# Optimization experiments

Measured on AMD Instinct MI355X. Metric: run time of the kernel, lower is better.

Reference implementation:

```python
import jax, jax.numpy as jnp
import numpy as np

H = 16  # num_heads
EPS = 1e-5


def _ln(x, g, b):
    m = x.mean(-1, keepdims=True)
    v = x.var(-1, keepdims=True)
    return (x - m) / jnp.sqrt(v + EPS) * g + b


def _heads(x):
    b, s, d = x.shape
    return x.reshape(b, s, H, d // H).transpose(0, 2, 1, 3)  # [B,H,S,dh]


def _merge_buggy(z):
    # replicate torch view([B,H,S,dh] -> [B,S,H*dh]) WITHOUT head transpose
    b, h, s, dh = z.shape
    return z.reshape(b, s, h * dh)


def _attn(q_in, kv_in, resid, wq, bq, wk, bk, wv, bv, g, be, scale_by_seq, apply_triu):
    q = _heads(q_in @ wq + bq)
    k = _heads(kv_in @ wk + bk)
    v = _heads(kv_in @ wv + bv)
    qk = jnp.einsum('bhqd,bhkd->bhqk', q, k)
    qk = jnp.where(jnp.isnan(qk), -jnp.inf, qk)
    if scale_by_seq:
        qk = qk / jnp.sqrt(jnp.asarray(qk.shape[-1], qk.dtype))  # sqrt(seq_len), as in source
    a = jax.nn.softmax(qk, axis=-1)
    a = jnp.where(jnp.isnan(a), 0.0, a)
    v = jnp.where(jnp.isnan(v), 0.0, v)
    if apply_triu:
        s = a.shape[-1]
        a = a * jnp.triu(jnp.ones((s, s), a.dtype))  # post-softmax multiplicative mask
    z = jnp.einsum('bhqk,bhkd->bhqd', a, v)
    z = _merge_buggy(z)
    return _ln(resid + z, g, be)


def setup_inputs() -> dict:
    key = jax.random.key(0)
    ks = jax.random.split(key, 20)
    B, S, D, F = 2, 2048, 1024, 1024
    p = lambda k, sh: (jax.random.normal(k, sh, jnp.float32) * 0.02)
    inp = {
        'encoded': jax.random.normal(ks[0], (B, S, D), jnp.float32),
        'decoded': jax.random.normal(ks[1], (B, S, D), jnp.float32),
        'sa_wq': p(ks[2], (D, D)), 'sa_bq': jnp.zeros((D,), jnp.float32),
        'sa_wk': p(ks[3], (D, D)), 'sa_bk': jnp.zeros((D,), jnp.float32),
        'sa_wv': p(ks[4], (D, D)), 'sa_bv': jnp.zeros((D,), jnp.float32),
        'sa_g': jnp.ones((D,), jnp.float32), 'sa_b': jnp.zeros((D,), jnp.float32),
        'ca_wq': p(ks[5], (D, D)), 'ca_bq': jnp.zeros((D,), jnp.float32),
        'ca_wk': p(ks[6], (D, D)), 'ca_bk': jnp.zeros((D,), jnp.float32),
        'ca_wv': p(ks[7], (D, D)), 'ca_bv': jnp.zeros((D,), jnp.float32),
        'ca_g': jnp.ones((D,), jnp.float32), 'ca_b': jnp.zeros((D,), jnp.float32),
        'ffn_w1': p(ks[8], (D, F)), 'ffn_b1': jnp.zeros((F,), jnp.float32),
        'ffn_w2': p(ks[9], (F, D)), 'ffn_b2': jnp.zeros((D,), jnp.float32),
        'ffn_g': jnp.ones((D,), jnp.float32), 'ffn_b': jnp.zeros((D,), jnp.float32),
    }
    return inp


def reference(encoded, decoded,
              sa_wq, sa_bq, sa_wk, sa_bk, sa_wv, sa_bv, sa_g, sa_b,
              ca_wq, ca_bq, ca_wk, ca_bk, ca_wv, ca_bv, ca_g, ca_b,
              ffn_w1, ffn_b1, ffn_w2, ffn_b2, ffn_g, ffn_b):
    # masked self-attention (quirky: scale by sqrt(S), post-softmax triu mask)
    x = _attn(decoded, decoded, decoded, sa_wq, sa_bq, sa_wk, sa_bk, sa_wv, sa_bv,
              sa_g, sa_b, scale_by_seq=True, apply_triu=True)
    # cross-attention (no scale, no mask)
    x = _attn(x, encoded, x, ca_wq, ca_bq, ca_wk, ca_bk, ca_wv, ca_bv,
              ca_g, ca_b, scale_by_seq=False, apply_triu=False)
    # FFN with residual + LayerNorm (dropout = identity in eval)
    y = jax.nn.relu(x @ ffn_w1 + ffn_b1) @ ffn_w2 + ffn_b2
    return _ln(y + x, ffn_g, ffn_b)
```

## Files before the change

### kernel.cpp

```cpp
#include <hip/hip_runtime.h>
#include <hip/hip_bf16.h>
#include <cstdint>


typedef __attribute__((ext_vector_type(8))) short bf16x8;
typedef __attribute__((ext_vector_type(4))) float f32x4;
typedef unsigned short u16;

#define MFMA16(a, b, c) __builtin_amdgcn_mfma_f32_16x16x32_bf16((a), (b), (c), 0, 0, 0)

__device__ __forceinline__ u16 f2b(float f) {
    __hip_bfloat16 h = __float2bfloat16(f);
    return __builtin_bit_cast(u16, h);
}
__device__ __forceinline__ float b2f(u16 u) {
    return __builtin_bit_cast(float, (uint32_t)u << 16);
}
__device__ __forceinline__ void g2lds16(const u16* g, u16* l) {
    __builtin_amdgcn_global_load_lds((const __attribute__((address_space(1))) void*)g,
                                     (__attribute__((address_space(3))) void*)l, 16, 0, 0);
}

__global__ __launch_bounds__(256) void cast_bf16_kernel(const float* __restrict__ x,
                                                        u16* __restrict__ y, int n4) {
    int i = blockIdx.x * 256 + threadIdx.x;
    if (i >= n4) return;
    float4 v = reinterpret_cast<const float4*>(x)[i];
    ushort4 o;
    o.x = f2b(v.x); o.y = f2b(v.y); o.z = f2b(v.z); o.w = f2b(v.w);
    reinterpret_cast<ushort4*>(y)[i] = o;
}

__global__ __launch_bounds__(256) void wcast_all_kernel(
    const float* __restrict__ w0, const float* __restrict__ w1,
    const float* __restrict__ w2, const float* __restrict__ w3,
    const float* __restrict__ w4, const float* __restrict__ w5,
    const float* __restrict__ w6, const float* __restrict__ w7,
    u16* __restrict__ wt) {
    __shared__ float t[32][33];
    const float* W;
    switch (blockIdx.z) {
        case 0: W = w0; break; case 1: W = w1; break;
        case 2: W = w2; break; case 3: W = w3; break;
        case 4: W = w4; break; case 5: W = w5; break;
        case 6: W = w6; break; default: W = w7; break;
    }
    u16* Wt = wt + (size_t)blockIdx.z * 1048576;
    int tx = threadIdx.x & 31, ty = threadIdx.x >> 5;
    int bx = blockIdx.x * 32, by = blockIdx.y * 32;
#pragma unroll
    for (int j = 0; j < 4; ++j)
        t[ty + j * 8][tx] = W[(size_t)(by + ty + j * 8) * 1024 + bx + tx];
    __syncthreads();
#pragma unroll
    for (int j = 0; j < 4; ++j)
        Wt[(size_t)(bx + ty + j * 8) * 1024 + by + tx] = f2b(t[tx][ty + j * 8]);
}

__global__ __launch_bounds__(256) void vtrans_kernel(const u16* __restrict__ V,
                                                     u16* __restrict__ Vt) {
    __shared__ u16 t[32][34];
    const int tx = threadIdx.x & 31, ty = threadIdx.x >> 5;
    const int s0 = blockIdx.x * 32, d0 = blockIdx.y * 32, b = blockIdx.z;
    const u16* src = V + (size_t)b * 2048 * 1024;
    u16* dst = Vt + (size_t)b * 1024 * 2048;
#pragma unroll
    for (int j = 0; j < 4; ++j)
        t[ty + j * 8][tx] = src[(size_t)(s0 + ty + j * 8) * 1024 + d0 + tx];
    __syncthreads();
#pragma unroll
    for (int j = 0; j < 4; ++j)
        dst[(size_t)(d0 + ty + j * 8) * 2048 + s0 + tx] = t[tx][ty + j * 8];
}

__global__ __launch_bounds__(256) void gemm_kernel(
    const u16* __restrict__ A, const u16* __restrict__ Bt,
    const float* __restrict__ bias0, const float* __restrict__ bias1,
    const float* __restrict__ bias2,
    u16* __restrict__ o0, u16* __restrict__ o1, u16* __restrict__ o2,
    int K, int relu, float oscale0) {
    __shared__ __align__(16) u16 As[2][128][32];
    __shared__ __align__(16) u16 Bs[2][128][32];
    const int tid = threadIdx.x, lane = tid & 63, w = tid >> 6;
    const int wm = w >> 1, wn = w & 1, l15 = lane & 15, l4 = lane >> 4;
    const int bm = blockIdx.y * 128, bn = blockIdx.x * 128;
    const int srow = lane >> 2, sc = lane & 3;
    const int scs = (sc ^ (srow & 3)) * 8;
    const u16* aW = A + (size_t)(bm + w * 16 + srow) * K + scs;
    const u16* bW = Bt + (size_t)(bn + w * 16 + srow) * K + scs;
    f32x4 acc[4][4] = {};

#define GSTAGE(bf, kt)                                                  \
    do {                                                                \
        g2lds16(aW + (kt), &As[bf][w * 16][0]);                         \
        g2lds16(aW + (size_t)64 * K + (kt), &As[bf][64 + w * 16][0]);   \
        g2lds16(bW + (kt), &Bs[bf][w * 16][0]);                         \
        g2lds16(bW + (size_t)64 * K + (kt), &Bs[bf][64 + w * 16][0]);   \
    } while (0)

    const int nt = K / 32;
    GSTAGE(0, 0);
    for (int t = 0; t < nt; ++t) {
        __syncthreads();
        if (t + 1 < nt) GSTAGE((t + 1) & 1, (t + 1) * 32);
        const int bf = t & 1;
        bf16x8 af[4], bfr[4];
#pragma unroll
        for (int m = 0; m < 4; ++m) {
            int row = wm * 64 + m * 16 + l15;
            af[m] = *reinterpret_cast<const bf16x8*>(&As[bf][row][(l4 ^ (l15 & 3)) * 8]);
        }
#pragma unroll
        for (int n = 0; n < 4; ++n) {
            int row = wn * 64 + n * 16 + l15;
            bfr[n] = *reinterpret_cast<const bf16x8*>(&Bs[bf][row][(l4 ^ (l15 & 3)) * 8]);
        }
        __builtin_amdgcn_s_setprio(1);
#pragma unroll
        for (int m = 0; m < 4; ++m)
#pragma unroll
            for (int n = 0; n < 4; ++n)
                acc[m][n] = MFMA16(af[m], bfr[n], acc[m][n]);
        __builtin_amdgcn_s_setprio(0);
    }
#undef GSTAGE
    const int which = bn >> 10;
    const float* bias = which == 0 ? bias0 : (which == 1 ? bias1 : bias2);
    u16* outp = which == 0 ? o0 : (which == 1 ? o1 : o2);
    const float osc = which == 0 ? oscale0 : 1.0f;
    const int bnl = bn & 1023;
#pragma unroll
    for (int m = 0; m < 4; ++m) {
#pragma unroll
        for (int n = 0; n < 4; ++n) {
            int col = bnl + wn * 64 + n * 16 + l15;
            float bv = bias[col];
            int row0 = bm + wm * 64 + m * 16 + l4 * 4;
#pragma unroll
            for (int r = 0; r < 4; ++r) {
                float v = (acc[m][n][r] + bv) * osc;
                if (relu) v = fmaxf(v, 0.f);
                outp[(size_t)(row0 + r) * 1024 + col] = f2b(v);
            }
        }
    }
}

template <int CAUSAL>
__global__ __launch_bounds__(256) void attn_kernel(const u16* __restrict__ Qb,
                                                   const u16* __restrict__ Kb,
                                                   const u16* __restrict__ Vt,
                                                   u16* __restrict__ Z) {
    const int S = 2048, D = 1024;
    __shared__ __align__(16) u16 Ks[2][64][64];
    __shared__ __align__(16) u16 Vs[2][64][64];
    __shared__ __align__(16) u16 Ps[4][16][72];
    const int tid = threadIdx.x, lane = tid & 63, w = tid >> 6;
    const int l15 = lane & 15, l4 = lane >> 4;
    const int hwid = blockIdx.x;
    const int wkid = (hwid & 7) * 128 + (hwid >> 3);
    const int qb = wkid & 31, h = (wkid >> 5) & 15, b = wkid >> 9;
    const int q0 = qb * 64 + w * 16;
    const int qg = q0 + l15;
    const size_t baseQ = (size_t)b * S * D + h * 64;
    const size_t baseVt = ((size_t)(b * 16 + h) * 64) * 2048;

    bf16x8 aq0, aq1;
    {
        const u16* qp = Qb + baseQ + (size_t)qg * D + l4 * 8;
        aq0 = *reinterpret_cast<const bf16x8*>(qp);
        aq1 = *reinterpret_cast<const bf16x8*>(qp + 32);
    }
    float lr = 0.f;
    f32x4 Oacc[4] = {};

    const int srow = lane >> 3, sc8 = lane & 7;
    const int scs = (sc8 ^ srow) * 8;
    const u16* kW = Kb + baseQ + (size_t)srow * D + scs;
    const u16* vW = Vt + baseVt + (size_t)srow * 2048 + scs;

#define KSTAGE(bf, t)                                                          \
    do {                                                                       \
        g2lds16(kW + (size_t)((t)*64 + (w * 2 + 0) * 8) * D, &Ks[bf][(w * 2 + 0) * 8][0]); \
        g2lds16(kW + (size_t)((t)*64 + (w * 2 + 1) * 8) * D, &Ks[bf][(w * 2 + 1) * 8][0]); \
    } while (0)
#define VSTAGE(bf, t)                                                          \
    do {                                                                       \
        g2lds16(vW + (size_t)((w * 2 + 0) * 8) * 2048 + (t)*64, &Vs[bf][(w * 2 + 0) * 8][0]); \
        g2lds16(vW + (size_t)((w * 2 + 1) * 8) * 2048 + (t)*64, &Vs[bf][(w * 2 + 1) * 8][0]); \
    } while (0)

    const int NT = S / 64;
    KSTAGE(0, 0);
    VSTAGE(0, 0);
    for (int t = 0; t < NT; ++t) {
        __syncthreads();
        const int bf = t & 1;
        if (t + 1 < NT) {
            KSTAGE((t + 1) & 1, t + 1);
            VSTAGE((t + 1) & 1, t + 1);
        }

        const f32x4 zero = {0.f, 0.f, 0.f, 0.f};
        float ts0 = 0.f, ts1 = 0.f, ts2 = 0.f, ts3 = 0.f;
        const bool maskTile = CAUSAL && (t * 64 < q0 + 16);
#pragma unroll
        for (int kg = 0; kg < 4; ++kg) {
            int kr = kg * 16 + l15;
            bf16x8 k0 = *reinterpret_cast<const bf16x8*>(&Ks[bf][kr][((0 + l4) ^ (l15 & 7)) * 8]);
            bf16x8 k1 = *reinterpret_cast<const bf16x8*>(&Ks[bf][kr][((4 + l4) ^ (l15 & 7)) * 8]);
            f32x4 sv = MFMA16(k0, aq0, zero);
            sv = MFMA16(k1, aq1, sv);
            float e0 = __builtin_exp2f(sv[0]);
            float e1 = __builtin_exp2f(sv[1]);
            float e2 = __builtin_exp2f(sv[2]);
            float e3 = __builtin_exp2f(sv[3]);
            ts0 += e0; ts1 += e1; ts2 += e2; ts3 += e3;
            if (maskTile) {
                int key = t * 64 + kg * 16 + l4 * 4;
                if (key + 0 < qg) e0 = 0.f;
                if (key + 1 < qg) e1 = 0.f;
                if (key + 2 < qg) e2 = 0.f;
                if (key + 3 < qg) e3 = 0.f;
            }
            ushort4 pw;
            pw.x = f2b(e0); pw.y = f2b(e1); pw.z = f2b(e2); pw.w = f2b(e3);
            *reinterpret_cast<ushort4*>(&Ps[w][l15][kg * 16 + l4 * 4]) = pw;
        }
        float es = (ts0 + ts1) + (ts2 + ts3);
        es += __shfl_xor(es, 16);
        es += __shfl_xor(es, 32);
        lr += es;

        bf16x8 vf[2][4];
#pragma unroll
        for (int kh = 0; kh < 2; ++kh)
#pragma unroll
            for (int n = 0; n < 4; ++n)
                vf[kh][n] = *reinterpret_cast<const bf16x8*>(
                    &Vs[bf][n * 16 + l15][((kh * 4 + l4) ^ (l15 & 7)) * 8]);

        asm volatile("s_waitcnt lgkmcnt(0)" ::: "memory");
        __builtin_amdgcn_sched_barrier(0);
        __builtin_amdgcn_s_setprio(1);
#pragma unroll
        for (int kh = 0; kh < 2; ++kh) {
            bf16x8 pa = *reinterpret_cast<const bf16x8*>(&Ps[w][l15][kh * 32 + l4 * 8]);
#pragma unroll
            for (int n = 0; n < 4; ++n) Oacc[n] = MFMA16(vf[kh][n], pa, Oacc[n]);
        }
        __builtin_amdgcn_s_setprio(0);
    }
#undef KSTAGE
#undef VSTAGE
    {
        float inv = 1.f / lr;
        int orow = h * 128 + (qg >> 4);
        int oc0 = (qg & 15) * 64;
#pragma unroll
        for (int n = 0; n < 4; ++n) {
            ushort4 o;
            o.x = f2b(Oacc[n][0] * inv); o.y = f2b(Oacc[n][1] * inv);
            o.z = f2b(Oacc[n][2] * inv); o.w = f2b(Oacc[n][3] * inv);
            *reinterpret_cast<ushort4*>(
                &Z[(size_t)b * S * D + (size_t)orow * D + oc0 + n * 16 + l4 * 4]) = o;
        }
    }
}

__global__ __launch_bounds__(256) void add_ln_kernel(const float* __restrict__ resid,
                                                     const u16* __restrict__ zb,
                                                     const float* __restrict__ g,
                                                     const float* __restrict__ bb,
                                                     float* __restrict__ outF,
                                                     u16* __restrict__ outH) {
    const int row = blockIdx.x * 4 + (threadIdx.x >> 6);
    const int lane = threadIdx.x & 63;
    const float* rp = resid + (size_t)row * 1024;
    const u16* zp = zb + (size_t)row * 1024;
    float v[16];
    float s = 0.f, s2 = 0.f;
#pragma unroll
    for (int k = 0; k < 4; ++k) {
        int col = k * 256 + lane * 4;
        float4 rv = *reinterpret_cast<const float4*>(rp + col);
        ushort4 zv = *reinterpret_cast<const ushort4*>(zp + col);
        float x0 = rv.x + b2f(zv.x);
        float x1 = rv.y + b2f(zv.y);
        float x2 = rv.z + b2f(zv.z);
        float x3 = rv.w + b2f(zv.w);
        v[k * 4 + 0] = x0; v[k * 4 + 1] = x1; v[k * 4 + 2] = x2; v[k * 4 + 3] = x3;
        s += x0 + x1 + x2 + x3;
        s2 += x0 * x0 + x1 * x1 + x2 * x2 + x3 * x3;
    }
#pragma unroll
    for (int o = 32; o >= 1; o >>= 1) {
        s += __shfl_xor(s, o);
        s2 += __shfl_xor(s2, o);
    }
    float mean = s * (1.f / 1024.f);
    float var = s2 * (1.f / 1024.f) - mean * mean;
    float rstd = rsqrtf(var + 1e-5f);
#pragma unroll
    for (int k = 0; k < 4; ++k) {
        int col = k * 256 + lane * 4;
        float4 gv = *reinterpret_cast<const float4*>(g + col);
        float4 bv = *reinterpret_cast<const float4*>(bb + col);
        float o0 = (v[k * 4 + 0] - mean) * rstd * gv.x + bv.x;
        float o1 = (v[k * 4 + 1] - mean) * rstd * gv.y + bv.y;
        float o2 = (v[k * 4 + 2] - mean) * rstd * gv.z + bv.z;
        float o3 = (v[k * 4 + 3] - mean) * rstd * gv.w + bv.w;
        if (outF) {
            float4 o = make_float4(o0, o1, o2, o3);
            *reinterpret_cast<float4*>(outF + (size_t)row * 1024 + col) = o;
        }
        if (outH) {
            ushort4 o;
            o.x = f2b(o0); o.y = f2b(o1); o.z = f2b(o2); o.w = f2b(o3);
            *reinterpret_cast<ushort4*>(outH + (size_t)row * 1024 + col) = o;
        }
    }
}

extern "C" void kernel_launch(void* const* d_in, const int* in_sizes, int n_in,
                              void* d_out, int out_size, void* d_ws, size_t ws_size,
                              hipStream_t stream) {
    const float* enc   = (const float*)d_in[0];
    const float* dec   = (const float*)d_in[1];
    const float* sa_wq = (const float*)d_in[2];  const float* sa_bq = (const float*)d_in[3];
    const float* sa_wk = (const float*)d_in[4];  const float* sa_bk = (const float*)d_in[5];
    const float* sa_wv = (const float*)d_in[6];  const float* sa_bv = (const float*)d_in[7];
    const float* sa_g  = (const float*)d_in[8];  const float* sa_b  = (const float*)d_in[9];
    const float* ca_wq = (const float*)d_in[10]; const float* ca_bq = (const float*)d_in[11];
    const float* ca_wk = (const float*)d_in[12]; const float* ca_bk = (const float*)d_in[13];
    const float* ca_wv = (const float*)d_in[14]; const float* ca_bv = (const float*)d_in[15];
    const float* ca_g  = (const float*)d_in[16]; const float* ca_b  = (const float*)d_in[17];
    const float* w1    = (const float*)d_in[18]; const float* b1    = (const float*)d_in[19];
    const float* w2    = (const float*)d_in[20]; const float* b2    = (const float*)d_in[21];
    const float* fg    = (const float*)d_in[22]; const float* fb    = (const float*)d_in[23];
    float* out = (float*)d_out;

    const int K = 1024;
    const size_t WSZ = 1048576;
    const size_t ASZ = 4194304;

    u16* wt   = (u16*)d_ws;
    u16* decB = wt + 8 * WSZ;
    u16* encB = decB + ASZ;
    u16* qB   = encB + ASZ;
    u16* kB   = qB + ASZ;
    u16* vB   = kB + ASZ;
    u16* zB   = vB + ASZ;
    float* x1f = (float*)(zB + ASZ);
    u16* xb   = (u16*)(x1f + ASZ);

    const float Q_SCALE_SELF = 0.031879354f;
    const float Q_SCALE_CROSS = 1.4426950408889634f;

    wcast_all_kernel<<<dim3(32, 32, 8), 256, 0, stream>>>(sa_wq, sa_wk, sa_wv, ca_wq,
                                                          ca_wk, ca_wv, w1, w2, wt);
    cast_bf16_kernel<<<4096, 256, 0, stream>>>(dec, decB, (int)(ASZ / 4));
    cast_bf16_kernel<<<4096, 256, 0, stream>>>(enc, encB, (int)(ASZ / 4));

    gemm_kernel<<<dim3(24, 32), 256, 0, stream>>>(decB, wt + 0 * WSZ,
                                                  sa_bq, sa_bk, sa_bv, qB, kB, vB, K, 0,
                                                  Q_SCALE_SELF);
    vtrans_kernel<<<dim3(64, 32, 2), 256, 0, stream>>>(vB, xb);
    attn_kernel<1><<<1024, 256, 0, stream>>>(qB, kB, xb, zB);
    add_ln_kernel<<<1024, 256, 0, stream>>>(dec, zB, sa_g, sa_b, x1f, xb);

    gemm_kernel<<<dim3(8, 32), 256, 0, stream>>>(xb, wt + 3 * WSZ,
                                                 ca_bq, ca_bq, ca_bq, qB, qB, qB, K, 0,
                                                 Q_SCALE_CROSS);
    gemm_kernel<<<dim3(16, 32), 256, 0, stream>>>(encB, wt + 4 * WSZ,
                                                  ca_bk, ca_bv, ca_bv, kB, vB, vB, K, 0,
                                                  1.0f);
    vtrans_kernel<<<dim3(64, 32, 2), 256, 0, stream>>>(vB, xb);
    attn_kernel<0><<<1024, 256, 0, stream>>>(qB, kB, xb, zB);
    add_ln_kernel<<<1024, 256, 0, stream>>>(x1f, zB, ca_g, ca_b, x1f, xb);

    gemm_kernel<<<dim3(8, 32), 256, 0, stream>>>(xb, wt + 6 * WSZ,
                                                 b1, b1, b1, qB, qB, qB, K, 1, 1.0f);
    gemm_kernel<<<dim3(8, 32), 256, 0, stream>>>(qB, wt + 7 * WSZ,
                                                 b2, b2, b2, zB, zB, zB, K, 0, 1.0f);
    add_ln_kernel<<<1024, 256, 0, stream>>>(x1f, zB, fg, fb, out, nullptr);
}
```

Baseline: 356.4 us.

## Skip masked PV tiles in causal attention and fuse cross-attn QKV GEMMs

In causal self-attention, the V tiles below the query block are no longer loaded, and their P·V MFMAs and P stores are skipped. The post-softmax triu mask zeroes those tiles, but the row sum still includes every key. The cross-attention Q projection and the K/V projections are merged into one GEMM launch that picks the A operand per column block. K is now hardcoded to 1024. This removes one launch and a large share of the causal PV work, at the cost of uneven per-block work and a less general GEMM.

```diff
diff --git a/kernel.cpp b/kernel.cpp
--- a/kernel.cpp
+++ b/kernel.cpp
@@ -74,20 +74,24 @@
 }
 
 __global__ __launch_bounds__(256) void gemm_kernel(
-    const u16* __restrict__ A, const u16* __restrict__ Bt,
+    const u16* __restrict__ A0, const u16* __restrict__ A1,
+    const u16* __restrict__ Btb,
     const float* __restrict__ bias0, const float* __restrict__ bias1,
     const float* __restrict__ bias2,
     u16* __restrict__ o0, u16* __restrict__ o1, u16* __restrict__ o2,
-    int K, int relu, float oscale0) {
+    int relu, float oscale0) {
+    const int K = 1024;
     __shared__ __align__(16) u16 As[2][128][32];
     __shared__ __align__(16) u16 Bs[2][128][32];
     const int tid = threadIdx.x, lane = tid & 63, w = tid >> 6;
     const int wm = w >> 1, wn = w & 1, l15 = lane & 15, l4 = lane >> 4;
     const int bm = blockIdx.y * 128, bn = blockIdx.x * 128;
+    const int which = bn >> 10;
+    const u16* A = (which == 0) ? A0 : A1;
     const int srow = lane >> 2, sc = lane & 3;
     const int scs = (sc ^ (srow & 3)) * 8;
     const u16* aW = A + (size_t)(bm + w * 16 + srow) * K + scs;
-    const u16* bW = Bt + (size_t)(bn + w * 16 + srow) * K + scs;
+    const u16* bW = Btb + (size_t)(bn + w * 16 + srow) * K + scs;
     f32x4 acc[4][4] = {};
 
 #define GSTAGE(bf, kt)                                                  \
@@ -124,7 +128,6 @@
         __builtin_amdgcn_s_setprio(0);
     }
 #undef GSTAGE
-    const int which = bn >> 10;
     const float* bias = which == 0 ? bias0 : (which == 1 ? bias1 : bias2);
     u16* outp = which == 0 ? o0 : (which == 1 ? o1 : o2);
     const float osc = which == 0 ? oscale0 : 1.0f;
@@ -191,19 +194,21 @@
     } while (0)
 
     const int NT = S / 64;
+    const int t0pv = CAUSAL ? qb : 0;
     KSTAGE(0, 0);
-    VSTAGE(0, 0);
+    if (0 >= t0pv) VSTAGE(0, 0);
     for (int t = 0; t < NT; ++t) {
         __syncthreads();
         const int bf = t & 1;
         if (t + 1 < NT) {
             KSTAGE((t + 1) & 1, t + 1);
-            VSTAGE((t + 1) & 1, t + 1);
-        }
+            if (t + 1 >= t0pv) VSTAGE((t + 1) & 1, t + 1);
+        }
+        const bool dopv = (t >= t0pv);
+        const bool maskT = CAUSAL && (t == qb);
 
         const f32x4 zero = {0.f, 0.f, 0.f, 0.f};
         float ts0 = 0.f, ts1 = 0.f, ts2 = 0.f, ts3 = 0.f;
-        const bool maskTile = CAUSAL && (t * 64 < q0 + 16);
 #pragma unroll
         for (int kg = 0; kg < 4; ++kg) {
             int kr = kg * 16 + l15;
@@ -216,40 +221,44 @@
             float e2 = __builtin_exp2f(sv[2]);
             float e3 = __builtin_exp2f(sv[3]);
             ts0 += e0; ts1 += e1; ts2 += e2; ts3 += e3;
-            if (maskTile) {
-                int key = t * 64 + kg * 16 + l4 * 4;
-                if (key + 0 < qg) e0 = 0.f;
-                if (key + 1 < qg) e1 = 0.f;
-                if (key + 2 < qg) e2 = 0.f;
-                if (key + 3 < qg) e3 = 0.f;
+            if (dopv) {
+                if (maskT) {
+                    int key = t * 64 + kg * 16 + l4 * 4;
+                    if (key + 0 < qg) e0 = 0.f;
+                    if (key + 1 < qg) e1 = 0.f;
+                    if (key + 2 < qg) e2 = 0.f;
+                    if (key + 3 < qg) e3 = 0.f;
+                }
+                ushort4 pw;
+                pw.x = f2b(e0); pw.y = f2b(e1); pw.z = f2b(e2); pw.w = f2b(e3);
+                *reinterpret_cast<ushort4*>(&Ps[w][l15][kg * 16 + l4 * 4]) = pw;
             }
-            ushort4 pw;
-            pw.x = f2b(e0); pw.y = f2b(e1); pw.z = f2b(e2); pw.w = f2b(e3);
-            *reinterpret_cast<ushort4*>(&Ps[w][l15][kg * 16 + l4 * 4]) = pw;
         }
         float es = (ts0 + ts1) + (ts2 + ts3);
         es += __shfl_xor(es, 16);
         es += __shfl_xor(es, 32);
         lr += es;
 
-        bf16x8 vf[2][4];
-#pragma unroll
-        for (int kh = 0; kh < 2; ++kh)
-#pragma unroll
-            for (int n = 0; n < 4; ++n)
-                vf[kh][n] = *reinterpret_cast<const bf16x8*>(
-                    &Vs[bf][n * 16 + l15][((kh * 4 + l4) ^ (l15 & 7)) * 8]);
-
-        asm volatile("s_waitcnt lgkmcnt(0)" ::: "memory");
-        __builtin_amdgcn_sched_barrier(0);
-        __builtin_amdgcn_s_setprio(1);
-#pragma unroll
-        for (int kh = 0; kh < 2; ++kh) {
-            bf16x8 pa = *reinterpret_cast<const bf16x8*>(&Ps[w][l15][kh * 32 + l4 * 8]);
-#pragma unroll
-            for (int n = 0; n < 4; ++n) Oacc[n] = MFMA16(vf[kh][n], pa, Oacc[n]);
-        }
-        __builtin_amdgcn_s_setprio(0);
+        if (dopv) {
+            bf16x8 vf[2][4];
+#pragma unroll
+            for (int kh = 0; kh < 2; ++kh)
+#pragma unroll
+                for (int n = 0; n < 4; ++n)
+                    vf[kh][n] = *reinterpret_cast<const bf16x8*>(
+                        &Vs[bf][n * 16 + l15][((kh * 4 + l4) ^ (l15 & 7)) * 8]);
+
+            asm volatile("s_waitcnt lgkmcnt(0)" ::: "memory");
+            __builtin_amdgcn_sched_barrier(0);
+            __builtin_amdgcn_s_setprio(1);
+#pragma unroll
+            for (int kh = 0; kh < 2; ++kh) {
+                bf16x8 pa = *reinterpret_cast<const bf16x8*>(&Ps[w][l15][kh * 32 + l4 * 8]);
+#pragma unroll
+                for (int n = 0; n < 4; ++n) Oacc[n] = MFMA16(vf[kh][n], pa, Oacc[n]);
+            }
+            __builtin_amdgcn_s_setprio(0);
+        }
     }
 #undef KSTAGE
 #undef VSTAGE
@@ -340,7 +349,6 @@
     const float* fg    = (const float*)d_in[22]; const float* fb    = (const float*)d_in[23];
     float* out = (float*)d_out;
 
-    const int K = 1024;
     const size_t WSZ = 1048576;
     const size_t ASZ = 4194304;
 
@@ -362,26 +370,23 @@
     cast_bf16_kernel<<<4096, 256, 0, stream>>>(dec, decB, (int)(ASZ / 4));
     cast_bf16_kernel<<<4096, 256, 0, stream>>>(enc, encB, (int)(ASZ / 4));
 
-    gemm_kernel<<<dim3(24, 32), 256, 0, stream>>>(decB, wt + 0 * WSZ,
-                                                  sa_bq, sa_bk, sa_bv, qB, kB, vB, K, 0,
-                                                  Q_SCALE_SELF);
+    gemm_kernel<<<dim3(24, 32), 256, 0, stream>>>(decB, decB, wt,
+                                                  sa_bq, sa_bk, sa_bv, qB, kB, vB,
+                                                  0, Q_SCALE_SELF);
     vtrans_kernel<<<dim3(64, 32, 2), 256, 0, stream>>>(vB, xb);
     attn_kernel<1><<<1024, 256, 0, stream>>>(qB, kB, xb, zB);
     add_ln_kernel<<<1024, 256, 0, stream>>>(dec, zB, sa_g, sa_b, x1f, xb);
 
-    gemm_kernel<<<dim3(8, 32), 256, 0, stream>>>(xb, wt + 3 * WSZ,
-                                                 ca_bq, ca_bq, ca_bq, qB, qB, qB, K, 0,
-                                                 Q_SCALE_CROSS);
-    gemm_kernel<<<dim3(16, 32), 256, 0, stream>>>(encB, wt + 4 * WSZ,
-                                                  ca_bk, ca_bv, ca_bv, kB, vB, vB, K, 0,
-                                                  1.0f);
+    gemm_kernel<<<dim3(24, 32), 256, 0, stream>>>(xb, encB, wt + 3 * WSZ,
+                                                  ca_bq, ca_bk, ca_bv, qB, kB, vB,
+                                                  0, Q_SCALE_CROSS);
     vtrans_kernel<<<dim3(64, 32, 2), 256, 0, stream>>>(vB, xb);
     attn_kernel<0><<<1024, 256, 0, stream>>>(qB, kB, xb, zB);
     add_ln_kernel<<<1024, 256, 0, stream>>>(x1f, zB, ca_g, ca_b, x1f, xb);
 
-    gemm_kernel<<<dim3(8, 32), 256, 0, stream>>>(xb, wt + 6 * WSZ,
-                                                 b1, b1, b1, qB, qB, qB, K, 1, 1.0f);
-    gemm_kernel<<<dim3(8, 32), 256, 0, stream>>>(qB, wt + 7 * WSZ,
-                                                 b2, b2, b2, zB, zB, zB, K, 0, 1.0f);
+    gemm_kernel<<<dim3(8, 32), 256, 0, stream>>>(xb, xb, wt + 6 * WSZ,
+                                                 b1, b1, b1, qB, qB, qB, 1, 1.0f);
+    gemm_kernel<<<dim3(8, 32), 256, 0, stream>>>(qB, qB, wt + 7 * WSZ,
+                                                 b2, b2, b2, zB, zB, zB, 0, 1.0f);
     add_ln_kernel<<<1024, 256, 0, stream>>>(x1f, zB, fg, fb, out, nullptr);
 }
```

Result: faster. 347.9 us (-2.4%).
